# Performance work log

Hardware: AMD Instinct MI355X
Metric: run time of the kernel (lower is better)

## Reference

```python
import jax, jax.numpy as jnp
import numpy as np

NEG = -1e9  # stand-in for -inf mask fill (avoids NaN, softmax weight ~0)
EPS = 1e-5  # torch LayerNorm default


def layer_norm(x, g, b):
    mu = jnp.mean(x, axis=-1, keepdims=True)
    var = jnp.mean(jnp.square(x - mu), axis=-1, keepdims=True)
    return (x - mu) * jax.lax.rsqrt(var + EPS) * g + b


def _forward(x, context, batch_lengths, max_len,
             Wq1, Wk1, Wv1, Wq2, Wk2, Wv2,
             ln1_g, ln1_b, ln2_g, ln2_b, ln3_g, ln3_b,
             fc1_w, fc1_b, fc2_w, fc2_b):
    B, L, E = x.shape
    H, _, dk = Wq1.shape
    pos = jnp.arange(L)
    valid = pos[None, :] < batch_lengths[:, None]                  # [B,L]
    out_mask = valid[:, :, None].astype(x.dtype)                   # [B,L,1] (outputMask)
    key_bias = jnp.where(valid, 0.0, NEG)[:, None, None, :]        # [B,1,1,L] (attnMask on keys)
    causal_bias = jnp.where(pos[:, None] >= pos[None, :], 0.0, NEG)  # [L,L] decoding mask
    scale = 1.0 / jnp.sqrt(jnp.asarray(dk, x.dtype))

    def mha(qk_src, v_src, Wq, Wk, Wv, causal):
        # Q,K from qk_src, V from v_src (faithful to Head.forward)
        m = out_mask[:, None]                                      # [B,1,L,1]
        Q = jnp.einsum('ble,hed->bhld', qk_src, Wq) * m
        K = jnp.einsum('ble,hed->bhld', qk_src, Wk) * m
        V = jnp.einsum('ble,hed->bhld', v_src, Wv) * m
        e = jnp.einsum('bhid,bhjd->bhij', Q, K) + key_bias
        if causal:
            e = e + causal_bias
        s = jax.nn.softmax(e * scale, axis=-1)
        o = jnp.einsum('bhij,bhjd->bhid', s, V)
        return o.transpose(0, 2, 1, 3).reshape(B, L, E)            # concat heads

    z = mha(x, x, Wq1, Wk1, Wv1, causal=True) * out_mask
    x1 = layer_norm(x + z, ln1_g, ln1_b)
    # cross block: Q,K from context, V from x1 (as in source)
    z = mha(context, x1, Wq2, Wk2, Wv2, causal=False) * out_mask
    x2 = layer_norm(x1 + z, ln2_g, ln2_b)
    h = jax.nn.relu(x2 @ fc1_w + fc1_b) * out_mask
    z = (h @ fc2_w + fc2_b) * out_mask
    return layer_norm(x2 + z, ln3_g, ln3_b)


def setup_inputs() -> dict:
    B, L, E, H = 8, 1024, 1024, 16
    dk = E // H
    key = jax.random.key(0)
    ks = jax.random.split(key, 16)
    w = lambda k, s: jax.random.normal(k, s, jnp.float32) * 0.02
    return {
        'x': jax.random.normal(ks[0], (B, L, E), jnp.float32),
        'context': jax.random.normal(ks[1], (B, L, E), jnp.float32),
        'batch_lengths': jax.random.randint(ks[2], (B,), 1, L + 1),
        'max_len': L,
        'Wq1': w(ks[3], (H, E, dk)), 'Wk1': w(ks[4], (H, E, dk)), 'Wv1': w(ks[5], (H, E, dk)),
        'Wq2': w(ks[6], (H, E, dk)), 'Wk2': w(ks[7], (H, E, dk)), 'Wv2': w(ks[8], (H, E, dk)),
        'ln1_g': jnp.ones((E,), jnp.float32), 'ln1_b': jnp.zeros((E,), jnp.float32),
        'ln2_g': jnp.ones((E,), jnp.float32), 'ln2_b': jnp.zeros((E,), jnp.float32),
        'ln3_g': jnp.ones((E,), jnp.float32), 'ln3_b': jnp.zeros((E,), jnp.float32),
        'fc1_w': w(ks[9], (E, E)), 'fc1_b': jnp.zeros((E,), jnp.float32),
        'fc2_w': w(ks[10], (E, E)), 'fc2_b': jnp.zeros((E,), jnp.float32),
    }


def reference(x, context, batch_lengths, max_len,
              Wq1, Wk1, Wv1, Wq2, Wk2, Wv2,
              ln1_g, ln1_b, ln2_g, ln2_b, ln3_g, ln3_b,
              fc1_w, fc1_b, fc2_w, fc2_b):
    return _forward(x, context, batch_lengths, max_len,
                    Wq1, Wk1, Wv1, Wq2, Wk2, Wv2,
                    ln1_g, ln1_b, ln2_g, ln2_b, ln3_g, ln3_b,
                    fc1_w, fc1_b, fc2_w, fc2_b)
```

## Files before the change

kernel.cpp:

```cpp
#include <hip/hip_runtime.h>


typedef unsigned short u16;
typedef unsigned int u32;
typedef __attribute__((ext_vector_type(8))) short bf16x8;
typedef __attribute__((ext_vector_type(4))) float f32x4;

#define Bv 8
#define Lv 1024
#define Ev 1024
#define Hv 16
#define DKv 64
#define Mv (Bv * Lv)

#if defined(__has_builtin)
# if __has_builtin(__builtin_amdgcn_global_load_lds)
#  define HAS_GLL 1
# endif
#endif
#ifndef HAS_GLL
# define HAS_GLL 0
#endif

#if HAS_GLL
__device__ __forceinline__ void gll16(const u16* g, u16* l) {
    __builtin_amdgcn_global_load_lds(
        (const __attribute__((address_space(1))) void*)(unsigned long long)(g),
        (__attribute__((address_space(3))) void*)(unsigned)(unsigned long long)(l),
        16, 0, 0);
}
#endif

__device__ __forceinline__ u16 f2bf(float f) {
    u32 u = __float_as_uint(f);
    u += 0x7fffu + ((u >> 16) & 1u);
    return (u16)(u >> 16);
}
__device__ __forceinline__ u32 pack2(float a, float b) {
    u32 ua = __float_as_uint(a); ua += 0x7fffu + ((ua >> 16) & 1u);
    u32 ub = __float_as_uint(b); ub += 0x7fffu + ((ub >> 16) & 1u);
    return (ua >> 16) | (ub & 0xffff0000u);
}
__device__ __forceinline__ float bf_lo(u32 u) { return __uint_as_float(u << 16); }
__device__ __forceinline__ float bf_hi(u32 u) { return __uint_as_float(u & 0xffff0000u); }

__global__ __launch_bounds__(256) void prep_k(
    const float* __restrict__ x, const float* __restrict__ ctx,
    const float* __restrict__ wq1, const float* __restrict__ wk1, const float* __restrict__ wv1,
    const float* __restrict__ wq2, const float* __restrict__ wk2, const float* __restrict__ wv2,
    const float* __restrict__ f1, const float* __restrict__ f2,
    u16* __restrict__ xb, u16* __restrict__ cb, u16* __restrict__ WT) {
    const int id = blockIdx.x, t = threadIdx.x;
    if (id < 16384) {
        const float* s = (id < 8192) ? x : ctx;
        u16* d = (id < 8192) ? xb : cb;
        const int i4 = ((id & 8191) * 256 + t) * 4;
        float4 v = *(const float4*)(s + i4);
        uint2 o = {pack2(v.x, v.y), pack2(v.z, v.w)};
        *(uint2*)(d + i4) = o;
        return;
    }
    __shared__ float tl[32][33];
    const int tx = t & 31, ty = t >> 5;
    if (id < 16384 + 6144) {
        const int wi = (id - 16384) >> 10;
        const int tile = (id - 16384) & 1023;
        const float* s = (wi == 0) ? wq1 : (wi == 1) ? wk1 : (wi == 2) ? wv1
                       : (wi == 3) ? wq2 : (wi == 4) ? wk2 : wv2;
        u16* d = WT + (size_t)wi * Ev * Ev;
        const int h = tile >> 6, rem = tile & 63;
        const int d0 = (rem & 1) * 32, e0 = (rem >> 1) * 32;
#pragma unroll
        for (int i = 0; i < 4; i++)
            tl[ty + i * 8][tx] = s[(size_t)h * Ev * DKv + (size_t)(e0 + ty + i * 8) * DKv + d0 + tx];
        __syncthreads();
#pragma unroll
        for (int i = 0; i < 4; i++)
            d[(size_t)(h * DKv + d0 + ty + i * 8) * Ev + e0 + tx] = f2bf(tl[tx][ty + i * 8]);
    } else {
        const int wi = (id - 16384 - 6144) >> 10;
        const int tile = (id - 16384 - 6144) & 1023;
        const float* s = wi ? f2 : f1;
        u16* d = WT + (size_t)(6 + wi) * Ev * Ev;
        const int n0 = (tile & 31) * 32, k0 = (tile >> 5) * 32;
#pragma unroll
        for (int i = 0; i < 4; i++)
            tl[ty + i * 8][tx] = s[(size_t)(k0 + ty + i * 8) * Ev + n0 + tx];
        __syncthreads();
#pragma unroll
        for (int i = 0; i < 4; i++)
            d[(size_t)(n0 + ty + i * 8) * Ev + k0 + tx] = f2bf(tl[tx][ty + i * 8]);
    }
}

template <int BIAS, int RELU, int TRANSW>
__global__ __launch_bounds__(256) void mgemm(const u16* __restrict__ A,
                                             const u16* __restrict__ Wt,
                                             const float* __restrict__ bias,
                                             u16* __restrict__ O0, u16* __restrict__ O1,
                                             u16* __restrict__ O2,
                                             const int* __restrict__ lens) {
    __shared__ u16 Alds[16 * 512];
    __shared__ u16 Blds[16 * 512];
    const int tid = threadIdx.x;
    const int w = tid >> 6, l = tid & 63;
    const int lc = l & 15, lq = l >> 4;
    const int row0 = blockIdx.y * 128, col0 = blockIdx.x * 128;
    const int which = col0 >> 10, colL = col0 & 1023;
    u16* C = (which == 0) ? O0 : (which == 1 ? O1 : O2);
    const bool tr = (TRANSW == which);

    int len = lens[row0 >> 10];
    len = min(max(len, 0), Lv);
    if ((row0 & (Lv - 1)) >= len) {
        const int rr = tid >> 1, cc = (tid & 1) * 64;
        u16* p = tr ? C + (size_t)(colL + rr) * Mv + row0 + cc
                    : C + (size_t)(row0 + rr) * Ev + colL + cc;
        uint4 z4 = {0u, 0u, 0u, 0u};
#pragma unroll
        for (int i = 0; i < 8; i++) *(uint4*)(p + i * 8) = z4;
        return;
    }

    const int wm4 = (w >> 1) * 4, wn4 = (w & 1) * 4;
    f32x4 acc[4][4];
#pragma unroll
    for (int i = 0; i < 4; i++)
#pragma unroll
        for (int j = 0; j < 4; j++) acc[i][j] = (f32x4){0.f, 0.f, 0.f, 0.f};

    const u16* Ag[4]; const u16* Bg[4]; u16* Al[4]; u16* Bl[4];
#pragma unroll
    for (int i = 0; i < 4; i++) {
        const int g16 = 2 * w + (i >> 1), k32 = i & 1;
        Ag[i] = A  + (size_t)(row0 + g16 * 16 + lc) * Ev + k32 * 32 + lq * 8;
        Bg[i] = Wt + (size_t)(col0 + g16 * 16 + lc) * Ev + k32 * 32 + lq * 8;
        Al[i] = Alds + (g16 * 2 + k32) * 512;
        Bl[i] = Blds + (g16 * 2 + k32) * 512;
    }

    for (int k0 = 0; k0 < Ev; k0 += 64) {
#if HAS_GLL
#pragma unroll
        for (int i = 0; i < 4; i++) { gll16(Ag[i], Al[i]); gll16(Bg[i], Bl[i]); }
#else
#pragma unroll
        for (int i = 0; i < 4; i++) {
            *(uint4*)(Al[i] + l * 8) = *(const uint4*)Ag[i];
            *(uint4*)(Bl[i] + l * 8) = *(const uint4*)Bg[i];
        }
#endif
#pragma unroll
        for (int i = 0; i < 4; i++) { Ag[i] += 64; Bg[i] += 64; }
        __syncthreads();
#pragma unroll
        for (int km = 0; km < 2; km++) {
            bf16x8 af[4], bfr[4];
#pragma unroll
            for (int mt = 0; mt < 4; mt++)
                af[mt] = *(const bf16x8*)(Alds + ((wm4 + mt) * 2 + km) * 512 + l * 8);
#pragma unroll
            for (int nt = 0; nt < 4; nt++)
                bfr[nt] = *(const bf16x8*)(Blds + ((wn4 + nt) * 2 + km) * 512 + l * 8);
#pragma unroll
            for (int mt = 0; mt < 4; mt++)
#pragma unroll
                for (int nt = 0; nt < 4; nt++)
                    acc[mt][nt] = __builtin_amdgcn_mfma_f32_16x16x32_bf16(
                        af[mt], bfr[nt], acc[mt][nt], 0, 0, 0);
        }
        __syncthreads();
    }

    float bv[4];
#pragma unroll
    for (int nt = 0; nt < 4; nt++)
        bv[nt] = BIAS ? bias[colL + wn4 * 16 + nt * 16 + lc] : 0.f;

#pragma unroll
    for (int mt = 0; mt < 4; mt++) {
        const int rowb = row0 + wm4 * 16 + mt * 16 + lq * 4;
#pragma unroll
        for (int nt = 0; nt < 4; nt++) {
            const int col = colL + wn4 * 16 + nt * 16 + lc;
            float v[4];
#pragma unroll
            for (int r = 0; r < 4; r++) {
                float xv = acc[mt][nt][r] + bv[nt];
                if (RELU) xv = fmaxf(xv, 0.f);
                v[r] = (((rowb + r) & (Lv - 1)) >= len) ? 0.f : xv;
            }
            if (tr) {
                uint2 o = {pack2(v[0], v[1]), pack2(v[2], v[3])};
                *(uint2*)(C + (size_t)col * Mv + rowb) = o;
            } else {
#pragma unroll
                for (int r = 0; r < 4; r++)
                    C[(size_t)(rowb + r) * Ev + col] = f2bf(v[r]);
            }
        }
    }
}

template <int CAUSAL>
__global__ __launch_bounds__(256) void mattn(u16* __restrict__ QZ,
                                             const u16* __restrict__ K,
                                             const u16* __restrict__ VT,
                                             const int* __restrict__ lens) {
    __shared__ u16 Kt[16 * 512];
    __shared__ u16 Vt[16 * 512];
    __shared__ u16 Pt[4 * 4 * 512];
    const int b = blockIdx.z, h = blockIdx.y, qb = blockIdx.x;
    const int q0 = qb * 128;
    const int tid = threadIdx.x;
    const int w = tid >> 6, l = tid & 63;
    const int lc = l & 15, lq = l >> 4;
    int len = lens[b];
    len = min(max(len, 0), Lv);

    if (q0 >= len) {
        const int zr = tid >> 1, zc = (tid & 1) * 32;
        uint4 z4 = {0u, 0u, 0u, 0u};
        uint4* p = (uint4*)(QZ + (size_t)(b * Lv + q0 + zr) * Ev + h * DKv + zc);
        p[0] = z4; p[1] = z4; p[2] = z4; p[3] = z4;
        return;
    }

    bf16x8 qf[2][2];
#pragma unroll
    for (int mt = 0; mt < 2; mt++)
#pragma unroll
        for (int k2 = 0; k2 < 2; k2++)
            qf[mt][k2] = *(const bf16x8*)(QZ + (size_t)(b * Lv + q0 + w * 32 + mt * 16 + lc) * Ev +
                                          h * DKv + k2 * 32 + lq * 8);

    f32x4 of[2][4];
#pragma unroll
    for (int mt = 0; mt < 2; mt++)
#pragma unroll
        for (int nd = 0; nd < 4; nd++) of[mt][nd] = (f32x4){0.f, 0.f, 0.f, 0.f};
    float mrow[2][4], lrow[2][4];
#pragma unroll
    for (int mt = 0; mt < 2; mt++)
#pragma unroll
        for (int r = 0; r < 4; r++) { mrow[mt][r] = -1e30f; lrow[mt][r] = 0.f; }

    const u16* Kg[4]; const u16* Vg[4]; u16* Kl[4]; u16* Vl[4];
#pragma unroll
    for (int i = 0; i < 4; i++) {
        const int k16 = 2 * w + (i >> 1), d32 = i & 1;
        Kg[i] = K + (size_t)(b * Lv + k16 * 16 + lc) * Ev + h * DKv + d32 * 32 + lq * 8;
        Kl[i] = Kt + (k16 * 2 + d32) * 512;
        Vg[i] = VT + (size_t)(h * DKv + w * 16 + lc) * Mv + b * Lv + i * 32 + lq * 8;
        Vl[i] = Vt + (w * 4 + i) * 512;
    }
    u16* Pw = Pt + w * 2048;

    const int jend = CAUSAL ? min(len, q0 + 128) : len;
    const int ntiles = (jend + 127) >> 7;

    for (int kt = 0; kt < ntiles; kt++) {
        const int koff = kt * 128;
#if HAS_GLL
#pragma unroll
        for (int i = 0; i < 4; i++) {
            gll16(Kg[i] + (size_t)koff * Ev, Kl[i]);
            gll16(Vg[i] + koff, Vl[i]);
        }
#else
#pragma unroll
        for (int i = 0; i < 4; i++) {
            *(uint4*)(Kl[i] + l * 8) = *(const uint4*)(Kg[i] + (size_t)koff * Ev);
            *(uint4*)(Vl[i] + l * 8) = *(const uint4*)(Vg[i] + koff);
        }
#endif
        __syncthreads();

        f32x4 sf[2][8];
#pragma unroll
        for (int nt = 0; nt < 8; nt++) {
            bf16x8 kf0 = *(const bf16x8*)(Kt + (nt * 2 + 0) * 512 + l * 8);
            bf16x8 kf1 = *(const bf16x8*)(Kt + (nt * 2 + 1) * 512 + l * 8);
#pragma unroll
            for (int mt = 0; mt < 2; mt++) {
                f32x4 s = (f32x4){0.f, 0.f, 0.f, 0.f};
                s = __builtin_amdgcn_mfma_f32_16x16x32_bf16(qf[mt][0], kf0, s, 0, 0, 0);
                s = __builtin_amdgcn_mfma_f32_16x16x32_bf16(qf[mt][1], kf1, s, 0, 0, 0);
                sf[mt][nt] = s;
            }
        }

        float alpha[2][4];
#pragma unroll
        for (int mt = 0; mt < 2; mt++) {
            float tmax[4] = {-1e30f, -1e30f, -1e30f, -1e30f};
#pragma unroll
            for (int nt = 0; nt < 8; nt++) {
                const int jj = koff + nt * 16 + lc;
                const bool jv = jj < len;
#pragma unroll
                for (int r = 0; r < 4; r++) {
                    const int iq = q0 + w * 32 + mt * 16 + lq * 4 + r;
                    const bool valid = jv && (!CAUSAL || jj <= iq);
                    float e = valid ? sf[mt][nt][r] * 0.125f : -1e30f;
                    sf[mt][nt][r] = e;
                    tmax[r] = fmaxf(tmax[r], e);
                }
            }
#pragma unroll
            for (int r = 0; r < 4; r++) {
#pragma unroll
                for (int d = 1; d < 16; d <<= 1)
                    tmax[r] = fmaxf(tmax[r], __shfl_xor(tmax[r], d, 64));
            }
            float psum[4];
#pragma unroll
            for (int r = 0; r < 4; r++) {
                const float mn = fmaxf(mrow[mt][r], tmax[r]);
                alpha[mt][r] = __expf(mrow[mt][r] - mn);
                mrow[mt][r] = mn;
                psum[r] = 0.f;
            }
#pragma unroll
            for (int nt = 0; nt < 8; nt++)
#pragma unroll
                for (int r = 0; r < 4; r++) {
                    float p = __expf(sf[mt][nt][r] - mrow[mt][r]);
                    sf[mt][nt][r] = p;
                    psum[r] += p;
                }
#pragma unroll
            for (int r = 0; r < 4; r++) {
#pragma unroll
                for (int d = 1; d < 16; d <<= 1) psum[r] += __shfl_xor(psum[r], d, 64);
                lrow[mt][r] = lrow[mt][r] * alpha[mt][r] + psum[r];
            }
#pragma unroll
            for (int nd = 0; nd < 4; nd++)
#pragma unroll
                for (int r = 0; r < 4; r++) of[mt][nd][r] *= alpha[mt][r];
        }

#pragma unroll
        for (int mt = 0; mt < 2; mt++) {
#pragma unroll
            for (int nt = 0; nt < 8; nt++)
#pragma unroll
                for (int r = 0; r < 4; r++)
                    Pw[(nt >> 1) * 512 +
                       ((2 * (nt & 1) + (lc >> 3)) * 16 + lq * 4 + r) * 8 + (lc & 7)] =
                        f2bf(sf[mt][nt][r]);
#pragma unroll
            for (int km = 0; km < 4; km++) {
                bf16x8 pa = *(const bf16x8*)(Pw + km * 512 + l * 8);
#pragma unroll
                for (int nd = 0; nd < 4; nd++) {
                    bf16x8 vb = *(const bf16x8*)(Vt + (nd * 4 + km) * 512 + l * 8);
                    of[mt][nd] = __builtin_amdgcn_mfma_f32_16x16x32_bf16(pa, vb, of[mt][nd], 0, 0, 0);
                }
            }
        }
        __syncthreads();
    }

#pragma unroll
    for (int mt = 0; mt < 2; mt++) {
        float inv[4];
#pragma unroll
        for (int r = 0; r < 4; r++) {
            const int iq = q0 + w * 32 + mt * 16 + lq * 4 + r;
            inv[r] = (iq < len && lrow[mt][r] > 0.f) ? (1.f / lrow[mt][r]) : 0.f;
        }
#pragma unroll
        for (int nd = 0; nd < 4; nd++)
#pragma unroll
            for (int r = 0; r < 4; r++)
                QZ[(size_t)(b * Lv + q0 + w * 32 + mt * 16 + lq * 4 + r) * Ev +
                   h * DKv + nd * 16 + lc] = f2bf(of[mt][nd][r] * inv[r]);
    }
}

template <int BASEBF, int OUTF32>
__global__ __launch_bounds__(256) void ln_k(const void* __restrict__ base,
                                            const u16* __restrict__ z,
                                            const float* __restrict__ g,
                                            const float* __restrict__ bta,
                                            void* __restrict__ out) {
    __shared__ float w1[4], w2[4];
    const int row = blockIdx.x, t = threadIdx.x;
    const int w = t >> 6, l = t & 63;
    const int c0 = t * 4;
    float v[4];
    if (BASEBF) {
        uint2 bu = *(const uint2*)((const u16*)base + (size_t)row * Ev + c0);
        v[0] = bf_lo(bu.x); v[1] = bf_hi(bu.x); v[2] = bf_lo(bu.y); v[3] = bf_hi(bu.y);
    } else {
        float4 f = *(const float4*)((const float*)base + (size_t)row * Ev + c0);
        v[0] = f.x; v[1] = f.y; v[2] = f.z; v[3] = f.w;
    }
    uint2 zu = *(const uint2*)(z + (size_t)row * Ev + c0);
    v[0] += bf_lo(zu.x); v[1] += bf_hi(zu.x); v[2] += bf_lo(zu.y); v[3] += bf_hi(zu.y);
    float s1 = v[0] + v[1] + v[2] + v[3];
    float s2 = v[0] * v[0] + v[1] * v[1] + v[2] * v[2] + v[3] * v[3];
#pragma unroll
    for (int d = 1; d < 64; d <<= 1) {
        s1 += __shfl_xor(s1, d, 64);
        s2 += __shfl_xor(s2, d, 64);
    }
    if (l == 0) { w1[w] = s1; w2[w] = s2; }
    __syncthreads();
    s1 = w1[0] + w1[1] + w1[2] + w1[3];
    s2 = w2[0] + w2[1] + w2[2] + w2[3];
    const float mu = s1 * (1.f / Ev);
    const float var = s2 * (1.f / Ev) - mu * mu;
    const float rinv = rsqrtf(fmaxf(var, 0.f) + 1e-5f);
    float4 gv = *(const float4*)(g + c0);
    float4 bv = *(const float4*)(bta + c0);
    float y[4];
    y[0] = (v[0] - mu) * rinv * gv.x + bv.x;
    y[1] = (v[1] - mu) * rinv * gv.y + bv.y;
    y[2] = (v[2] - mu) * rinv * gv.z + bv.z;
    y[3] = (v[3] - mu) * rinv * gv.w + bv.w;
    if (OUTF32) {
        float4 ow = {y[0], y[1], y[2], y[3]};
        *(float4*)((float*)out + (size_t)row * Ev + c0) = ow;
    } else {
        uint2 ow = {pack2(y[0], y[1]), pack2(y[2], y[3])};
        *(uint2*)((u16*)out + (size_t)row * Ev + c0) = ow;
    }
}

extern "C" void kernel_launch(void* const* d_in, const int* in_sizes, int n_in,
                              void* d_out, int out_size, void* d_ws, size_t ws_size,
                              hipStream_t stream) {
    const float* x    = (const float*)d_in[0];
    const float* ctx  = (const float*)d_in[1];
    const int*   lens = (const int*)d_in[2];
    const float* Wq1 = (const float*)d_in[4];
    const float* Wk1 = (const float*)d_in[5];
    const float* Wv1 = (const float*)d_in[6];
    const float* Wq2 = (const float*)d_in[7];
    const float* Wk2 = (const float*)d_in[8];
    const float* Wv2 = (const float*)d_in[9];
    const float* g1 = (const float*)d_in[10], *b1 = (const float*)d_in[11];
    const float* g2 = (const float*)d_in[12], *b2 = (const float*)d_in[13];
    const float* g3 = (const float*)d_in[14], *b3 = (const float*)d_in[15];
    const float* fc1w = (const float*)d_in[16], *fc1b = (const float*)d_in[17];
    const float* fc2w = (const float*)d_in[18], *fc2b = (const float*)d_in[19];

    const size_t WSZ = (size_t)Ev * Ev;
    const size_t MM  = (size_t)Mv * Ev;
    u16* WT = (u16*)d_ws;
    u16* Wtq1 = WT + 0 * WSZ;
    u16* Wtq2 = WT + 3 * WSZ, *Wtv2 = WT + 5 * WSZ;
    u16* Wtf1 = WT + 6 * WSZ, *Wtf2 = WT + 7 * WSZ;
    u16* B1 = WT + 8 * WSZ;
    u16* B2 = B1 + MM;
    u16* B3 = B2 + MM;
    u16* B4 = B3 + MM;
    u16* xb = (u16*)d_out;
    u16* cb = xb + MM;

    dim3 gP(24576), gQKV(24, 64), gQK(16, 64), gG1(8, 64), gA(8, Hv, Bv), gL(Mv);

    prep_k<<<gP, 256, 0, stream>>>(x, ctx, Wq1, Wk1, Wv1, Wq2, Wk2, Wv2, fc1w, fc2w,
                                   xb, cb, WT);

    mgemm<0, 0, 2><<<gQKV, 256, 0, stream>>>(xb, Wtq1, nullptr, B1, B2, B3, lens);
    mattn<1><<<gA, 256, 0, stream>>>(B1, B2, B3, lens);
    ln_k<0, 0><<<gL, 256, 0, stream>>>(x, B1, g1, b1, B2);

    mgemm<0, 0, -1><<<gQK, 256, 0, stream>>>(cb, Wtq2, nullptr, B1, B3, nullptr, lens);
    mgemm<0, 0, 0><<<gG1, 256, 0, stream>>>(B2, Wtv2, nullptr, B4, nullptr, nullptr, lens);
    mattn<0><<<gA, 256, 0, stream>>>(B1, B3, B4, lens);
    ln_k<1, 0><<<gL, 256, 0, stream>>>(B2, B1, g2, b2, B3);

    mgemm<1, 1, -1><<<gG1, 256, 0, stream>>>(B3, Wtf1, fc1b, B1, nullptr, nullptr, lens);
    mgemm<1, 0, -1><<<gG1, 256, 0, stream>>>(B1, Wtf2, fc2b, B2, nullptr, nullptr, lens);
    ln_k<1, 1><<<gL, 256, 0, stream>>>(B3, B2, g3, b3, d_out);
}
```

Before: 566.9 us.

## Double-buffer LDS tiles in GEMM and attention kernels to overlap loads with MFMA

Both the projection GEMM and the flash-attention kernel now keep two LDS buffers for the A/B (or K/V) tiles. The first tile is loaded before the loop, and each iteration issues the next tile's loads into the alternate buffer before running MFMAs on the current one. This aims to hide global-memory latency behind compute and removes one barrier per iteration. In exchange it doubles the per-block LDS footprint (64KB for the GEMM, 80KB for attention), which may reduce how many blocks fit on each CU. It also depends on the barrier waiting for the async global-to-LDS loads to finish.

```diff
diff --git a/kernel.cpp b/kernel.cpp
--- a/kernel.cpp
+++ b/kernel.cpp
@@ -100,8 +100,8 @@
                                              u16* __restrict__ O0, u16* __restrict__ O1,
                                              u16* __restrict__ O2,
                                              const int* __restrict__ lens) {
-    __shared__ u16 Alds[16 * 512];
-    __shared__ u16 Blds[16 * 512];
+    __shared__ u16 Alds[2][16 * 512];
+    __shared__ u16 Blds[2][16 * 512];
     const int tid = threadIdx.x;
     const int w = tid >> 6, l = tid & 63;
     const int lc = l & 15, lq = l >> 4;
@@ -129,39 +129,57 @@
 #pragma unroll
         for (int j = 0; j < 4; j++) acc[i][j] = (f32x4){0.f, 0.f, 0.f, 0.f};
 
-    const u16* Ag[4]; const u16* Bg[4]; u16* Al[4]; u16* Bl[4];
+    const u16* Ag[4]; const u16* Bg[4];
+    int lof[4];
 #pragma unroll
     for (int i = 0; i < 4; i++) {
         const int g16 = 2 * w + (i >> 1), k32 = i & 1;
         Ag[i] = A  + (size_t)(row0 + g16 * 16 + lc) * Ev + k32 * 32 + lq * 8;
         Bg[i] = Wt + (size_t)(col0 + g16 * 16 + lc) * Ev + k32 * 32 + lq * 8;
-        Al[i] = Alds + (g16 * 2 + k32) * 512;
-        Bl[i] = Blds + (g16 * 2 + k32) * 512;
-    }
-
+        lof[i] = (g16 * 2 + k32) * 512;
+    }
+
+#if HAS_GLL
+#pragma unroll
+    for (int i = 0; i < 4; i++) { gll16(Ag[i], &Alds[0][lof[i]]); gll16(Bg[i], &Blds[0][lof[i]]); }
+#else
+#pragma unroll
+    for (int i = 0; i < 4; i++) {
+        *(uint4*)(&Alds[0][lof[i] + l * 8]) = *(const uint4*)Ag[i];
+        *(uint4*)(&Blds[0][lof[i] + l * 8]) = *(const uint4*)Bg[i];
+    }
+#endif
+    __syncthreads();
+
+    int cur = 0;
     for (int k0 = 0; k0 < Ev; k0 += 64) {
+        if (k0 + 64 < Ev) {
+            const int koff = k0 + 64;
 #if HAS_GLL
 #pragma unroll
-        for (int i = 0; i < 4; i++) { gll16(Ag[i], Al[i]); gll16(Bg[i], Bl[i]); }
+            for (int i = 0; i < 4; i++) {
+                gll16(Ag[i] + koff, &Alds[cur ^ 1][lof[i]]);
+                gll16(Bg[i] + koff, &Blds[cur ^ 1][lof[i]]);
+            }
 #else
 #pragma unroll
-        for (int i = 0; i < 4; i++) {
-            *(uint4*)(Al[i] + l * 8) = *(const uint4*)Ag[i];
-            *(uint4*)(Bl[i] + l * 8) = *(const uint4*)Bg[i];
-        }
-#endif
-#pragma unroll
-        for (int i = 0; i < 4; i++) { Ag[i] += 64; Bg[i] += 64; }
-        __syncthreads();
+            for (int i = 0; i < 4; i++) {
+                *(uint4*)(&Alds[cur ^ 1][lof[i] + l * 8]) = *(const uint4*)(Ag[i] + koff);
+                *(uint4*)(&Blds[cur ^ 1][lof[i] + l * 8]) = *(const uint4*)(Bg[i] + koff);
+            }
+#endif
+        }
+        const u16* Ab = &Alds[cur][0];
+        const u16* Bb = &Blds[cur][0];
 #pragma unroll
         for (int km = 0; km < 2; km++) {
             bf16x8 af[4], bfr[4];
 #pragma unroll
             for (int mt = 0; mt < 4; mt++)
-                af[mt] = *(const bf16x8*)(Alds + ((wm4 + mt) * 2 + km) * 512 + l * 8);
+                af[mt] = *(const bf16x8*)(Ab + ((wm4 + mt) * 2 + km) * 512 + l * 8);
 #pragma unroll
             for (int nt = 0; nt < 4; nt++)
-                bfr[nt] = *(const bf16x8*)(Blds + ((wn4 + nt) * 2 + km) * 512 + l * 8);
+                bfr[nt] = *(const bf16x8*)(Bb + ((wn4 + nt) * 2 + km) * 512 + l * 8);
 #pragma unroll
             for (int mt = 0; mt < 4; mt++)
 #pragma unroll
@@ -170,6 +188,7 @@
                         af[mt], bfr[nt], acc[mt][nt], 0, 0, 0);
         }
         __syncthreads();
+        cur ^= 1;
     }
 
     float bv[4];
@@ -207,8 +226,8 @@
                                              const u16* __restrict__ K,
                                              const u16* __restrict__ VT,
                                              const int* __restrict__ lens) {
-    __shared__ u16 Kt[16 * 512];
-    __shared__ u16 Vt[16 * 512];
+    __shared__ u16 Kt[2][16 * 512];
+    __shared__ u16 Vt[2][16 * 512];
     __shared__ u16 Pt[4 * 4 * 512];
     const int b = blockIdx.z, h = blockIdx.y, qb = blockIdx.x;
     const int q0 = qb * 128;
@@ -245,42 +264,63 @@
 #pragma unroll
         for (int r = 0; r < 4; r++) { mrow[mt][r] = -1e30f; lrow[mt][r] = 0.f; }
 
-    const u16* Kg[4]; const u16* Vg[4]; u16* Kl[4]; u16* Vl[4];
+    const u16* Kg[4]; const u16* Vg[4];
+    int kof[4], vof[4];
 #pragma unroll
     for (int i = 0; i < 4; i++) {
         const int k16 = 2 * w + (i >> 1), d32 = i & 1;
         Kg[i] = K + (size_t)(b * Lv + k16 * 16 + lc) * Ev + h * DKv + d32 * 32 + lq * 8;
-        Kl[i] = Kt + (k16 * 2 + d32) * 512;
+        kof[i] = (k16 * 2 + d32) * 512;
         Vg[i] = VT + (size_t)(h * DKv + w * 16 + lc) * Mv + b * Lv + i * 32 + lq * 8;
-        Vl[i] = Vt + (w * 4 + i) * 512;
+        vof[i] = (w * 4 + i) * 512;
     }
     u16* Pw = Pt + w * 2048;
 
     const int jend = CAUSAL ? min(len, q0 + 128) : len;
     const int ntiles = (jend + 127) >> 7;
 
+#if HAS_GLL
+#pragma unroll
+    for (int i = 0; i < 4; i++) {
+        gll16(Kg[i], &Kt[0][kof[i]]);
+        gll16(Vg[i], &Vt[0][vof[i]]);
+    }
+#else
+#pragma unroll
+    for (int i = 0; i < 4; i++) {
+        *(uint4*)(&Kt[0][kof[i] + l * 8]) = *(const uint4*)Kg[i];
+        *(uint4*)(&Vt[0][vof[i] + l * 8]) = *(const uint4*)Vg[i];
+    }
+#endif
+    __syncthreads();
+
+    int cur = 0;
     for (int kt = 0; kt < ntiles; kt++) {
         const int koff = kt * 128;
+        if (kt + 1 < ntiles) {
+            const int knext = koff + 128;
 #if HAS_GLL
 #pragma unroll
-        for (int i = 0; i < 4; i++) {
-            gll16(Kg[i] + (size_t)koff * Ev, Kl[i]);
-            gll16(Vg[i] + koff, Vl[i]);
-        }
+            for (int i = 0; i < 4; i++) {
+                gll16(Kg[i] + (size_t)knext * Ev, &Kt[cur ^ 1][kof[i]]);
+                gll16(Vg[i] + knext, &Vt[cur ^ 1][vof[i]]);
+            }
 #else
 #pragma unroll
-        for (int i = 0; i < 4; i++) {
-            *(uint4*)(Kl[i] + l * 8) = *(const uint4*)(Kg[i] + (size_t)koff * Ev);
-            *(uint4*)(Vl[i] + l * 8) = *(const uint4*)(Vg[i] + koff);
-        }
-#endif
-        __syncthreads();
+            for (int i = 0; i < 4; i++) {
+                *(uint4*)(&Kt[cur ^ 1][kof[i] + l * 8]) = *(const uint4*)(Kg[i] + (size_t)knext * Ev);
+                *(uint4*)(&Vt[cur ^ 1][vof[i] + l * 8]) = *(const uint4*)(Vg[i] + knext);
+            }
+#endif
+        }
+        const u16* Kb = &Kt[cur][0];
+        const u16* Vb = &Vt[cur][0];
 
         f32x4 sf[2][8];
 #pragma unroll
         for (int nt = 0; nt < 8; nt++) {
-            bf16x8 kf0 = *(const bf16x8*)(Kt + (nt * 2 + 0) * 512 + l * 8);
-            bf16x8 kf1 = *(const bf16x8*)(Kt + (nt * 2 + 1) * 512 + l * 8);
+            bf16x8 kf0 = *(const bf16x8*)(Kb + (nt * 2 + 0) * 512 + l * 8);
+            bf16x8 kf1 = *(const bf16x8*)(Kb + (nt * 2 + 1) * 512 + l * 8);
 #pragma unroll
             for (int mt = 0; mt < 2; mt++) {
                 f32x4 s = (f32x4){0.f, 0.f, 0.f, 0.f};
@@ -355,12 +395,13 @@
                 bf16x8 pa = *(const bf16x8*)(Pw + km * 512 + l * 8);
 #pragma unroll
                 for (int nd = 0; nd < 4; nd++) {
-                    bf16x8 vb = *(const bf16x8*)(Vt + (nd * 4 + km) * 512 + l * 8);
+                    bf16x8 vb = *(const bf16x8*)(Vb + (nd * 4 + km) * 512 + l * 8);
                     of[mt][nd] = __builtin_amdgcn_mfma_f32_16x16x32_bf16(pa, vb, of[mt][nd], 0, 0, 0);
                 }
             }
         }
         __syncthreads();
+        cur ^= 1;
     }
 
 #pragma unroll
```

After: 533.7 us. -5.9%, faster.
